# Kernel tuning notes

Hardware: AMD Instinct MI355X
Metric: run time of the kernel (lower is better)

The kernel has to match this reference:

```python
import jax, jax.numpy as jnp
import numpy as np

N_NODES = 4096
HID = 64
N_STEP = 10
_OFFSETS = np.array([1, 2, 5, 11, 23, 47, 97, 193])  # circulant graph -> degree 16


def setup_inputs() -> dict:
    rng = np.random.default_rng(0)
    N = N_NODES
    i = np.repeat(np.arange(N), len(_OFFSETS))
    j = (i + np.tile(_OFFSETS, N)) % N
    vals = rng.normal(0.0, 0.5, i.shape).astype(np.float32)
    J = np.zeros((N, N), np.float32)
    J[i, j] = vals
    J[j, i] = vals  # symmetric coupling matrix
    row, col = np.nonzero(J)                      # E directed edges, row-major sorted
    key_fwd = row.astype(np.int64) * N + col
    rev = np.searchsorted(key_fwd, col.astype(np.int64) * N + row)  # reverse-edge index
    ru, cu = np.nonzero(np.triu(J))               # Eu upper-triangular edges
    u2e = np.searchsorted(key_fwd, ru.astype(np.int64) * N + cu)    # upper -> full edge index
    bias = rng.normal(0.0, 0.5, N).astype(np.float32)
    p = lambda *s: jnp.asarray(rng.normal(0.0, 0.1, s).astype(np.float32))
    return {
        'J': jnp.asarray(J), 'bias': jnp.asarray(bias),
        'gat_W': p(4, HID), 'gat_a': p(2 * HID, 1),
        'ci_W1': p(4, HID), 'ci_b1': jnp.zeros((HID,), jnp.float32),
        'ci_W2': p(HID, HID), 'ci_b2': jnp.zeros((HID,), jnp.float32),
        'ci_W3': p(HID, 1), 'ci_b3': jnp.zeros((1,), jnp.float32),
        'row': jnp.asarray(row.astype(np.int32)), 'col': jnp.asarray(col.astype(np.int32)),
        'rev': jnp.asarray(rev.astype(np.int32)),
        'ru': jnp.asarray(ru.astype(np.int32)), 'cu': jnp.asarray(cu.astype(np.int32)),
        'u2e': jnp.asarray(u2e.astype(np.int32)),
        'N_step': N_STEP, 'MPNNtype': 0,
    }


def reference(J, bias, gat_W, gat_a, ci_W1, ci_b1, ci_W2, ci_b2, ci_W3, ci_b3,
              row, col, rev, ru, cu, u2e, N_step, MPNNtype):
    N = J.shape[0]
    adj = (jnp.abs(J) > 0).astype(J.dtype)
    # node features: [-b, b, degree, row-sum of J]
    feat = jnp.stack([-bias, bias, adj.sum(1), J.sum(1)], axis=1)  # [N,4]
    # GAT scores: e[i,j] = leakyrelu([Wh_i || Wh_j] @ a) = leakyrelu(Wh_i@a1 + Wh_j@a2)
    Wh = feat @ gat_W                                  # [N,H]
    f1 = Wh @ gat_a[:HID, 0]
    f2 = Wh @ gat_a[HID:, 0]
    e = jax.nn.leaky_relu(f1[:, None] + f2[None, :], 0.2)
    att = jnp.where(adj > 0, jnp.exp(e), 0.0)
    Cij_matrix = 0.5 * (att + att.T)                   # [N,N]
    Cij_e = Cij_matrix[row, col]                       # [E]
    # Ci readout MLP
    h = jax.nn.relu(feat @ ci_W1 + ci_b1)
    h = jax.nn.relu(h @ ci_W2 + ci_b2)
    Ci = h @ ci_W3 + ci_b3                             # [N,1]
    dom = Ci + Cij_matrix.sum(1, keepdims=True)
    dom = jnp.sign(dom) * jnp.maximum(jnp.abs(dom), 0.1)  # clamp |.| >= 0.1
    bias_scale = bias / dom[:, 0]
    bx_scale = jnp.stack([-bias_scale, bias_scale], axis=1)  # [N,2]
    Jv = J[row, col]
    Jxy_scale = jnp.stack([jnp.stack([Jv, -Jv], -1),
                           jnp.stack([-Jv, Jv], -1)], axis=1) / Cij_e[:, None, None]  # [E,2,2]

    def node_update(em):
        # node_messages[j,:] = sum over edges (i->j) of em[e,:]
        nm = jax.ops.segment_sum(em, col, num_segments=N) / dom   # [N,2]
        lnZ = jnp.log(jnp.sum(jnp.exp(bx_scale + nm), axis=1, keepdims=True))
        return bx_scale + nm - lnZ, lnZ

    em0 = jnp.zeros((row.shape[0], 2), J.dtype)  # log of all-ones messages
    hidden0, lnZ0 = node_update(em0)

    def bp_step(carry, _):
        em, hidden, lnZ = carry
        ln_pj = hidden[row][:, :, None]     # [E,2,1]
        ln_zj = lnZ[row][:, :, None]        # [E,1,1]
        ln_mu_ij = em[rev][:, :, None]      # message on reverse edge, [E,2,1]
        M = jnp.exp(Jxy_scale + ln_pj + ln_zj - ln_mu_ij)          # [E,2,2]
        M = M / jnp.sum(jnp.max(M, axis=1), axis=1)[:, None, None]
        em_new = jnp.log(jnp.max(M ** Cij_e[:, None, None], axis=1))  # [E,2]
        hidden_new, lnZ_new = node_update(em_new)
        return (em_new, hidden_new, lnZ_new), None

    (em, hidden, lnZ), _ = jax.lax.scan(bp_step, (em0, hidden0, lnZ0), None, length=N_step)

    readout = jnp.exp(hidden)                           # [N,2]
    Js = J[ru, cu] / Cij_matrix[ru, cu]                 # [Eu]
    Jxy_u = jnp.exp(jnp.stack([jnp.stack([Js, -Js], -1),
                               jnp.stack([-Js, Js], -1)], axis=1))  # [Eu,2,2]
    temp_i = readout[cu] / jnp.exp(em[u2e])             # [Eu,2]
    temp_j = readout[ru] / jnp.exp(em[rev[u2e]])        # [Eu,2]
    pw = Jxy_u * temp_i[:, None, :] * temp_j[:, :, None]
    pw = pw / jnp.sum(pw, axis=(1, 2), keepdims=True)
    readout_pairwise = pw.reshape(-1, 4)                # [Eu,4]
    Cij_u = Cij_matrix[ru, cu]
    node_H = -jnp.sum(readout * jnp.log(readout + 1e-16), axis=1)
    edge_H = -jnp.sum(readout_pairwise * jnp.log(readout_pairwise + 1e-16), axis=1)
    node_entropy = Ci[:, 0] @ jax.lax.stop_gradient(node_H)
    edge_entropy = Cij_u @ jax.lax.stop_gradient(edge_H)
    return (readout, readout_pairwise, node_entropy + edge_entropy,
            node_entropy, edge_entropy, Ci[:, 0], Cij_u, dom)
```

## Files before the change

kernel.cpp:

```cpp
#include <hip/hip_runtime.h>
#include <cstddef>

#define TB    512
#define NB    128
#define NSTEP 10
#define SENTV 0xFFFFFFFFFFFFFFFFULL

__device__ __forceinline__ float lse2(float a, float b) {
    return fmaxf(a, b) + __logf(1.0f + __expf(-fabsf(a - b)));
}

__device__ __forceinline__ void stA(float2* p, float2 v) {
    union { float2 f; unsigned long long u; } x; x.f = v;
    __hip_atomic_store((unsigned long long*)p, x.u,
                       __ATOMIC_RELAXED, __HIP_MEMORY_SCOPE_AGENT);
}
__device__ __forceinline__ float2 pollLd(const float2* p) {
    union { float2 f; unsigned long long u; } x;
    x.u = __hip_atomic_load((const unsigned long long*)p,
                            __ATOMIC_RELAXED, __HIP_MEMORY_SCOPE_AGENT);
    while (x.u == SENTV) {
        __builtin_amdgcn_s_sleep(1);
        x.u = __hip_atomic_load((const unsigned long long*)p,
                                __ATOMIC_RELAXED, __HIP_MEMORY_SCOPE_AGENT);
    }
    return x.f;
}

struct KParams {
    const float *J, *bias, *gat_W, *gat_a, *W1, *b1, *W2, *b2, *W3, *b3;
    const int *col, *rev, *ru, *cu, *u2e;
    int N, Eu;
    float2 *fAIn, *jsC, *em, *uIn, *uFin;
    float  *ci_out, *dom_out, *ent;
    float2* ro_out;
    float4* rp_out;
    float*  cij_out;
};

__global__ __launch_bounds__(TB) void k_fused(KParams p) {
    __shared__ float4 sW2T[64 * 17];
    __shared__ float  sh1[TB / 16][68];
    __shared__ float  red[TB / 64];

    const int tidb = threadIdx.x;
    const int g = blockIdx.x * TB + tidb;
    const int i = g >> 4, t = g & 15;
    const int lane = tidb & 63;
    const int E = p.N * 16;

    for (int idx = tidb; idx < 64 * 16; idx += TB) {
        const int o = idx >> 4, hh = idx & 15;
        sW2T[o * 17 + hh] = make_float4(
            p.W2[(4 * hh + 0) * 64 + o], p.W2[(4 * hh + 1) * 64 + o],
            p.W2[(4 * hh + 2) * 64 + o], p.W2[(4 * hh + 3) * 64 + o]);
    }
    if (g < 3) {
        __hip_atomic_store((int*)&p.ent[g], 0,
                           __ATOMIC_RELAXED, __HIP_MEMORY_SCOPE_AGENT);
    }

    const int j  = p.col[g];
    const int rg = p.rev[g];
    const float Jv = p.J[(size_t)i * (size_t)p.N + (size_t)j];

    float rs = Jv;
    rs += __shfl_xor(rs, 1); rs += __shfl_xor(rs, 2);
    rs += __shfl_xor(rs, 4); rs += __shfl_xor(rs, 8);

    const float bi = p.bias[i];

    float s8 = 0.0f;
    {
        const int d8 = lane >> 3, c8 = lane & 7;
        const int kk = d8 & 3;
        const float* ga = p.gat_a + ((d8 < 4) ? 0 : 64);
        #pragma unroll
        for (int h = 0; h < 8; ++h)
            s8 += p.gat_W[kk * 64 + 8 * c8 + h] * ga[8 * c8 + h];
        s8 += __shfl_xor(s8, 1); s8 += __shfl_xor(s8, 2); s8 += __shfl_xor(s8, 4);
    }
    const float w10 = __shfl(s8, 0),  w11 = __shfl(s8, 8);
    const float w12 = __shfl(s8, 16), w13 = __shfl(s8, 24);
    const float w20 = __shfl(s8, 32), w21 = __shfl(s8, 40);
    const float w22 = __shfl(s8, 48), w23 = __shfl(s8, 56);
    const float fd = 16.0f;
    const float f1i = -bi * w10 + bi * w11 + fd * w12 + rs * w13;
    const float f2i = -bi * w20 + bi * w21 + fd * w22 + rs * w23;
    stA(&p.fAIn[rg], make_float2(f1i, f2i));

    const int nib = tidb >> 4;
    #pragma unroll
    for (int m = 0; m < 4; ++m) {
        int h = t + 16 * m;
        float a = -bi * p.W1[h] + bi * p.W1[64 + h] + fd * p.W1[128 + h]
                + rs * p.W1[192 + h] + p.b1[h];
        sh1[nib][h] = fmaxf(a, 0.0f);
    }
    __syncthreads();
    float4 hv[16];
    {
        const float4* hrow = (const float4*)&sh1[nib][0];
        #pragma unroll
        for (int hh = 0; hh < 16; ++hh) hv[hh] = hrow[hh];
    }
    float civ = 0.0f;
    #pragma unroll
    for (int m = 0; m < 4; ++m) {
        const int o = t + 16 * m;
        const float4* wrow = &sW2T[o * 17];
        float acc = p.b2[o];
        #pragma unroll
        for (int hh = 0; hh < 16; ++hh) {
            const float4 wv = wrow[hh];
            acc += hv[hh].x * wv.x + hv[hh].y * wv.y
                 + hv[hh].z * wv.z + hv[hh].w * wv.w;
        }
        civ += fmaxf(acc, 0.0f) * p.W3[o];
    }
    civ += __shfl_xor(civ, 1); civ += __shfl_xor(civ, 2);
    civ += __shfl_xor(civ, 4); civ += __shfl_xor(civ, 8);
    const float ci = civ + p.b3[0];

    const float2 fj = pollLd(&p.fAIn[g]);
    float x1 = f1i + fj.y; x1 = (x1 > 0.0f) ? x1 : 0.2f * x1;
    float x2 = fj.x + f2i; x2 = (x2 > 0.0f) ? x2 : 0.2f * x2;
    const float C  = 0.5f * (__expf(x1) + __expf(x2));
    const float js = Jv / C;
    stA(&p.jsC[g], make_float2(js, C));

    float sc = C;
    sc += __shfl_xor(sc, 1); sc += __shfl_xor(sc, 2);
    sc += __shfl_xor(sc, 4); sc += __shfl_xor(sc, 8);
    const float s  = ci + sc;
    const float cl = fmaxf(fabsf(s), 0.1f);
    const float d  = (s > 0.0f) ? cl : ((s < 0.0f) ? -cl : 0.0f);
    const float rd = 1.0f / d;
    const float bs = bi * rd;
    if (t == 0) {
        p.ci_out[i] = ci;
        p.dom_out[i] = d;
    }
    stA(&p.uIn[rg], make_float2(-bs, bs));

    int eE = 0, eR = 0, eC = 0, eEr = 0;
    if (g < p.Eu) {
        eE = p.u2e[g]; eR = p.ru[g]; eC = p.cu[g];
        eEr = p.rev[eE];
    }

    float in0 = 0.0f, in1 = 0.0f;
    float out0 = 0.0f, out1 = 0.0f;
    float ui0 = -bs, ui1 = bs;
    for (int st = 0; st < NSTEP; ++st) {
        const float2 uj = pollLd(&p.uIn[(size_t)st * E + g]);
        const float a0 = uj.x - out0, a1 = uj.y - out1;
        const float t0 = fmaxf( js + a0, -js + a1);
        const float t1 = fmaxf(-js + a0,  js + a1);
        const float ls = lse2(t0, t1);
        const float ni0 = C * (t0 - ls), ni1 = C * (t1 - ls);
        const float pu0 = ui0, pu1 = ui1;
        const float pi0 = in0, pi1 = in1;
        in0 = ni0; in1 = ni1;

        float nm0 = in0, nm1 = in1;
        nm0 += __shfl_xor(nm0, 1); nm1 += __shfl_xor(nm1, 1);
        nm0 += __shfl_xor(nm0, 2); nm1 += __shfl_xor(nm1, 2);
        nm0 += __shfl_xor(nm0, 4); nm1 += __shfl_xor(nm1, 4);
        nm0 += __shfl_xor(nm0, 8); nm1 += __shfl_xor(nm1, 8);
        ui0 = -bs + nm0 * rd; ui1 = bs + nm1 * rd;
        if (st < NSTEP - 1) {
            stA(&p.uIn[(size_t)(st + 1) * E + rg], make_float2(ui0, ui1));
        } else {
            if (t == 0) stA(&p.uFin[i], make_float2(ui0, ui1));
            stA(&p.em[g], make_float2(in0, in1));
        }

        const float b0 = pu0 - pi0, b1 = pu1 - pi1;
        const float q0 = fmaxf( js + b0, -js + b1);
        const float q1 = fmaxf(-js + b0,  js + b1);
        const float qs = lse2(q0, q1);
        out0 = C * (q0 - qs); out1 = C * (q1 - qs);
    }

    float nodeC = 0.0f;
    if (t == 0) {
        const float lz = lse2(ui0, ui1);
        const float r0 = __expf(ui0 - lz), r1 = __expf(ui1 - lz);
        p.ro_out[i] = make_float2(r0, r1);
        const float H = -(r0 * __logf(r0 + 1e-16f) + r1 * __logf(r1 + 1e-16f));
        nodeC = ci * H;
    }
    for (int off = 32; off > 0; off >>= 1) nodeC += __shfl_down(nodeC, off);
    {
        const int wv = tidb >> 6;
        if (lane == 0) red[wv] = nodeC;
        __syncthreads();
        if (tidb == 0) {
            float sn = 0.0f;
            #pragma unroll
            for (int w = 0; w < TB / 64; ++w) sn += red[w];
            atomicAdd(&p.ent[0], sn);
            atomicAdd(&p.ent[1], sn);
        }
        __syncthreads();
    }

    float edgeC = 0.0f;
    if (g < p.Eu) {
        const float2 jc = pollLd(&p.jsC[eE]);
        const float jse = jc.x, Ce = jc.y;
        const float2 uc = pollLd(&p.uFin[eC]), ur = pollLd(&p.uFin[eR]);
        const float2 eme = pollLd(&p.em[eEr]);
        const float2 emr = pollLd(&p.em[eE]);
        const float lc = lse2(uc.x, uc.y);
        const float lr = lse2(ur.x, ur.y);
        const float ti0 = (uc.x - lc) - eme.x, ti1 = (uc.y - lc) - eme.y;
        const float tj0 = (ur.x - lr) - emr.x, tj1 = (ur.y - lr) - emr.y;
        const float L00 =  jse + ti0 + tj0;
        const float L01 = -jse + ti1 + tj0;
        const float L10 = -jse + ti0 + tj1;
        const float L11 =  jse + ti1 + tj1;
        const float mL = fmaxf(fmaxf(L00, L01), fmaxf(L10, L11));
        float p00 = __expf(L00 - mL), p01 = __expf(L01 - mL);
        float p10 = __expf(L10 - mL), p11 = __expf(L11 - mL);
        const float inv = 1.0f / (p00 + p01 + p10 + p11);
        p00 *= inv; p01 *= inv; p10 *= inv; p11 *= inv;
        p.rp_out[g] = make_float4(p00, p01, p10, p11);
        p.cij_out[g] = Ce;
        const float H = -(p00 * __logf(p00 + 1e-16f) + p01 * __logf(p01 + 1e-16f)
                        + p10 * __logf(p10 + 1e-16f) + p11 * __logf(p11 + 1e-16f));
        edgeC = Ce * H;
    }
    for (int off = 32; off > 0; off >>= 1) edgeC += __shfl_down(edgeC, off);
    const int wv = tidb >> 6;
    if (lane == 0) red[wv] = edgeC;
    __syncthreads();
    if (tidb == 0) {
        float se = 0.0f;
        #pragma unroll
        for (int w = 0; w < TB / 64; ++w) se += red[w];
        atomicAdd(&p.ent[0], se);
        atomicAdd(&p.ent[2], se);
    }
}

extern "C" void kernel_launch(void* const* d_in, const int* in_sizes, int n_in,
                              void* d_out, int out_size, void* d_ws, size_t ws_size,
                              hipStream_t stream) {
    const int N  = in_sizes[1];
    const int E  = in_sizes[10];
    const int Eu = in_sizes[13];

    float* out = (float*)d_out;
    size_t OFF_RP  = 2 * (size_t)N;
    size_t OFF_ENT = OFF_RP + 4 * (size_t)Eu;

    char* w = (char*)d_ws;
    auto carve = [&](size_t bytes) {
        void* q = (void*)w;
        w += (bytes + 255) & ~(size_t)255;
        return q;
    };

    KParams p;
    p.J     = (const float*)d_in[0];
    p.bias  = (const float*)d_in[1];
    p.gat_W = (const float*)d_in[2];
    p.gat_a = (const float*)d_in[3];
    p.W1    = (const float*)d_in[4];
    p.b1    = (const float*)d_in[5];
    p.W2    = (const float*)d_in[6];
    p.b2    = (const float*)d_in[7];
    p.W3    = (const float*)d_in[8];
    p.b3    = (const float*)d_in[9];
    p.col   = (const int*)d_in[11];
    p.rev   = (const int*)d_in[12];
    p.ru    = (const int*)d_in[13];
    p.cu    = (const int*)d_in[14];
    p.u2e   = (const int*)d_in[15];
    p.N = N; p.Eu = Eu;

    const size_t szFA = (size_t)E * 8;
    const size_t szJC = (size_t)E * 8;
    const size_t szEM = (size_t)E * 8;
    const size_t szUI = (size_t)NSTEP * E * 8;
    const size_t szUF = (size_t)N * 8;
    p.fAIn = (float2*)carve(szFA);
    p.jsC  = (float2*)carve(szJC);
    p.em   = (float2*)carve(szEM);
    p.uIn  = (float2*)carve(szUI);
    p.uFin = (float2*)carve(szUF);

    p.ro_out  = (float2*)out;
    p.rp_out  = (float4*)(out + OFF_RP);
    p.ent     = out + OFF_ENT;
    p.ci_out  = p.ent + 3;
    p.cij_out = p.ci_out + N;
    p.dom_out = p.cij_out + Eu;

    hipMemsetAsync(p.fAIn, 0xFF, szFA + szJC + szEM + szUI + szUF, stream);
    k_fused<<<dim3(NB), dim3(TB), 0, stream>>>(p);
}
```

Measured before the change: 157.1 us.

## Recompute neighbor GAT features locally and batch final readout polls

Result: slower. 167.8 us (+6.8%).

```diff
diff --git a/kernel.cpp b/kernel.cpp
--- a/kernel.cpp
+++ b/kernel.cpp
@@ -15,14 +15,16 @@
     __hip_atomic_store((unsigned long long*)p, x.u,
                        __ATOMIC_RELAXED, __HIP_MEMORY_SCOPE_AGENT);
 }
+__device__ __forceinline__ unsigned long long ldU(const float2* p) {
+    return __hip_atomic_load((const unsigned long long*)p,
+                             __ATOMIC_RELAXED, __HIP_MEMORY_SCOPE_AGENT);
+}
 __device__ __forceinline__ float2 pollLd(const float2* p) {
     union { float2 f; unsigned long long u; } x;
-    x.u = __hip_atomic_load((const unsigned long long*)p,
-                            __ATOMIC_RELAXED, __HIP_MEMORY_SCOPE_AGENT);
+    x.u = ldU(p);
     while (x.u == SENTV) {
         __builtin_amdgcn_s_sleep(1);
-        x.u = __hip_atomic_load((const unsigned long long*)p,
-                                __ATOMIC_RELAXED, __HIP_MEMORY_SCOPE_AGENT);
+        x.u = ldU(p);
     }
     return x.f;
 }
@@ -31,7 +33,7 @@
     const float *J, *bias, *gat_W, *gat_a, *W1, *b1, *W2, *b2, *W3, *b3;
     const int *col, *rev, *ru, *cu, *u2e;
     int N, Eu;
-    float2 *fAIn, *jsC, *em, *uIn, *uFin;
+    float2 *jsC, *em, *uIn, *uFin;
     float  *ci_out, *dom_out, *ent;
     float2* ro_out;
     float4* rp_out;
@@ -62,13 +64,19 @@
 
     const int j  = p.col[g];
     const int rg = p.rev[g];
-    const float Jv = p.J[(size_t)i * (size_t)p.N + (size_t)j];
-
-    float rs = Jv;
-    rs += __shfl_xor(rs, 1); rs += __shfl_xor(rs, 2);
-    rs += __shfl_xor(rs, 4); rs += __shfl_xor(rs, 8);
-
-    const float bi = p.bias[i];
+    const float* Jri = p.J + (size_t)i * (size_t)p.N;
+    const float* Jrj = p.J + (size_t)j * (size_t)p.N;
+    const int* coli = p.col + 16 * i;
+    const int* colj = p.col + 16 * j;
+    const float Jv = Jri[j];
+
+    float rs = 0.0f, rsj = 0.0f;
+    #pragma unroll 4
+    for (int tt = 0; tt < 16; ++tt) rs  += Jri[coli[tt]];
+    #pragma unroll 4
+    for (int tt = 0; tt < 16; ++tt) rsj += Jrj[colj[tt]];
+
+    const float bi = p.bias[i], bj = p.bias[j];
 
     float s8 = 0.0f;
     {
@@ -85,9 +93,20 @@
     const float w20 = __shfl(s8, 32), w21 = __shfl(s8, 40);
     const float w22 = __shfl(s8, 48), w23 = __shfl(s8, 56);
     const float fd = 16.0f;
-    const float f1i = -bi * w10 + bi * w11 + fd * w12 + rs * w13;
-    const float f2i = -bi * w20 + bi * w21 + fd * w22 + rs * w23;
-    stA(&p.fAIn[rg], make_float2(f1i, f2i));
+    const float f1i = -bi * w10 + bi * w11 + fd * w12 + rs  * w13;
+    const float f2i = -bi * w20 + bi * w21 + fd * w22 + rs  * w23;
+    const float f1j = -bj * w10 + bj * w11 + fd * w12 + rsj * w13;
+    const float f2j = -bj * w20 + bj * w21 + fd * w22 + rsj * w23;
+
+    float x1 = f1i + f2j; x1 = (x1 > 0.0f) ? x1 : 0.2f * x1;
+    float x2 = f1j + f2i; x2 = (x2 > 0.0f) ? x2 : 0.2f * x2;
+    const float C  = 0.5f * (__expf(x1) + __expf(x2));
+    const float js = Jv / C;
+    stA(&p.jsC[g], make_float2(js, C));
+
+    float sc = C;
+    sc += __shfl_xor(sc, 1); sc += __shfl_xor(sc, 2);
+    sc += __shfl_xor(sc, 4); sc += __shfl_xor(sc, 8);
 
     const int nib = tidb >> 4;
     #pragma unroll
@@ -122,16 +141,6 @@
     civ += __shfl_xor(civ, 4); civ += __shfl_xor(civ, 8);
     const float ci = civ + p.b3[0];
 
-    const float2 fj = pollLd(&p.fAIn[g]);
-    float x1 = f1i + fj.y; x1 = (x1 > 0.0f) ? x1 : 0.2f * x1;
-    float x2 = fj.x + f2i; x2 = (x2 > 0.0f) ? x2 : 0.2f * x2;
-    const float C  = 0.5f * (__expf(x1) + __expf(x2));
-    const float js = Jv / C;
-    stA(&p.jsC[g], make_float2(js, C));
-
-    float sc = C;
-    sc += __shfl_xor(sc, 1); sc += __shfl_xor(sc, 2);
-    sc += __shfl_xor(sc, 4); sc += __shfl_xor(sc, 8);
     const float s  = ci + sc;
     const float cl = fmaxf(fabsf(s), 0.1f);
     const float d  = (s > 0.0f) ? cl : ((s < 0.0f) ? -cl : 0.0f);
@@ -208,11 +217,28 @@
 
     float edgeC = 0.0f;
     if (g < p.Eu) {
-        const float2 jc = pollLd(&p.jsC[eE]);
-        const float jse = jc.x, Ce = jc.y;
-        const float2 uc = pollLd(&p.uFin[eC]), ur = pollLd(&p.uFin[eR]);
-        const float2 eme = pollLd(&p.em[eEr]);
-        const float2 emr = pollLd(&p.em[eE]);
+        const float2* A0 = &p.jsC[eE];
+        const float2* A1 = &p.em[eE];
+        const float2* A2 = &p.em[eEr];
+        const float2* A3 = &p.uFin[eR];
+        const float2* A4 = &p.uFin[eC];
+        union { float2 f; unsigned long long u; } a0, a1, a2, a3, a4;
+        a0.u = a1.u = a2.u = a3.u = a4.u = SENTV;
+        for (;;) {
+            if (a0.u == SENTV) a0.u = ldU(A0);
+            if (a1.u == SENTV) a1.u = ldU(A1);
+            if (a2.u == SENTV) a2.u = ldU(A2);
+            if (a3.u == SENTV) a3.u = ldU(A3);
+            if (a4.u == SENTV) a4.u = ldU(A4);
+            if (a0.u != SENTV && a1.u != SENTV && a2.u != SENTV &&
+                a3.u != SENTV && a4.u != SENTV) break;
+            __builtin_amdgcn_s_sleep(1);
+        }
+        const float jse = a0.f.x, Ce = a0.f.y;
+        const float2 emr = a1.f;
+        const float2 eme = a2.f;
+        const float2 ur  = a3.f;
+        const float2 uc  = a4.f;
         const float lc = lse2(uc.x, uc.y);
         const float lr = lse2(ur.x, ur.y);
         const float ti0 = (uc.x - lc) - eme.x, ti1 = (uc.y - lc) - eme.y;
@@ -281,12 +307,10 @@
     p.u2e   = (const int*)d_in[15];
     p.N = N; p.Eu = Eu;
 
-    const size_t szFA = (size_t)E * 8;
     const size_t szJC = (size_t)E * 8;
     const size_t szEM = (size_t)E * 8;
     const size_t szUI = (size_t)NSTEP * E * 8;
     const size_t szUF = (size_t)N * 8;
-    p.fAIn = (float2*)carve(szFA);
     p.jsC  = (float2*)carve(szJC);
     p.em   = (float2*)carve(szEM);
     p.uIn  = (float2*)carve(szUI);
@@ -299,6 +323,6 @@
     p.cij_out = p.ci_out + N;
     p.dom_out = p.cij_out + Eu;
 
-    hipMemsetAsync(p.fAIn, 0xFF, szFA + szJC + szEM + szUI + szUF, stream);
+    hipMemsetAsync(p.jsC, 0xFF, szJC + szEM + szUI + szUF, stream);
     k_fused<<<dim3(NB), dim3(TB), 0, stream>>>(p);
 }
```
